# Kernel tuning notes

Measured on AMD Instinct MI355X. Metric: run time of the kernel, lower is better.

The kernel has to match this reference:

```python
import jax, jax.numpy as jnp
import numpy as np

N_NODES = 50000
N_EDGES = 600000
DIMS = [128, 128, 128]  # input_dim + hidden_dims


def setup_inputs() -> dict:
    key = jax.random.key(0)
    ks = jax.random.split(key, 8)
    node_features = jax.random.normal(ks[0], (N_NODES, DIMS[0]), dtype=jnp.float32)
    edge_index = jax.random.randint(ks[1], (2, N_EDGES), 0, N_NODES, dtype=jnp.int64)
    # GCNConv params: weight [in, out] (glorot-ish), bias [out] (zeros init in PyG; use small randn)
    W1 = jax.random.normal(ks[2], (DIMS[0], DIMS[1]), dtype=jnp.float32) / np.sqrt(DIMS[0])
    b1 = jnp.zeros((DIMS[1],), dtype=jnp.float32)
    W2 = jax.random.normal(ks[3], (DIMS[1], DIMS[2]), dtype=jnp.float32) / np.sqrt(DIMS[1])
    b2 = jnp.zeros((DIMS[2],), dtype=jnp.float32)
    return {"node_features": node_features, "edge_index": edge_index,
            "W1": W1, "b1": b1, "W2": W2, "b2": b2}


def _gcn_norm(edge_index, n_nodes):
    # Add self loops, then symmetric normalization as in PyG gcn_norm.
    loop = jnp.arange(n_nodes, dtype=edge_index.dtype)
    src = jnp.concatenate([edge_index[0], loop])  # message sources (x_j)
    dst = jnp.concatenate([edge_index[1], loop])  # aggregation targets
    deg = jax.ops.segment_sum(jnp.ones_like(dst, dtype=jnp.float32), dst,
                              num_segments=n_nodes)
    dinv = jnp.where(deg > 0, jax.lax.rsqrt(jnp.maximum(deg, 1.0)), 0.0)
    norm = dinv[src] * dinv[dst]  # [E + N]
    return src, dst, norm


def _gcn_layer(x, W, b, src, dst, norm, n_nodes):
    h = x @ W                                  # [N, out]
    msgs = h[src] * norm[:, None]              # gather + scale  [E+N, out]
    out = jax.ops.segment_sum(msgs, dst, num_segments=n_nodes)  # scatter-add
    return out + b


def reference(node_features, edge_index, W1, b1, W2, b2):
    n_nodes = node_features.shape[0]
    src, dst, norm = _gcn_norm(edge_index, n_nodes)
    x = _gcn_layer(node_features, W1, b1, src, dst, norm, n_nodes)
    x = jax.nn.relu(x)  # ReLU between layers, none after last
    x = _gcn_layer(x, W2, b2, src, dst, norm, n_nodes)
    return x
```

## Files before the change

### kernel.cpp

```cpp
#include <hip/hip_runtime.h>
#include <hip/hip_bf16.h>

typedef __bf16 bf16_t;
typedef __bf16 bf16x8 __attribute__((ext_vector_type(8)));
typedef float f32x4 __attribute__((ext_vector_type(4)));
typedef unsigned short u16;

#define DIM 128
#define CAPE 62

__global__ void k_prep(const float* __restrict__ W1, const float* __restrict__ W2,
                       bf16_t* __restrict__ TH1, bf16_t* __restrict__ TL1,
                       bf16_t* __restrict__ TH2, bf16_t* __restrict__ TL2) {
    int b = blockIdx.x;
    const float* W = (b == 0) ? W1 : W2;
    bf16_t* TH = (b == 0) ? TH1 : TH2;
    bf16_t* TL = (b == 0) ? TL1 : TL2;
    for (int idx = threadIdx.x; idx < 128 * 128; idx += 256) {
        int j    = idx & 7;
        int lane = (idx >> 3) & 63;
        int kc   = (idx >> 9) & 3;
        int nt   = idx >> 11;
        int nn = nt * 16 + (lane & 15);
        int k  = kc * 32 + (lane >> 4) * 8 + j;
        float wv = W[k * 128 + nn];
        bf16_t h = (bf16_t)wv;
        TH[idx] = h;
        TL[idx] = (bf16_t)(wv - (float)h);
    }
}

__global__ __launch_bounds__(256) void k_front(
        const bf16_t* __restrict__ TH1, const bf16_t* __restrict__ TL1,
        const float* __restrict__ A, bf16_t* __restrict__ H, int M, int SB,
        const int* __restrict__ EI, int* __restrict__ ell, int e) {
    int b = blockIdx.x;
    int tid = threadIdx.x;
    if (b < SB) {
        __shared__ int any;
        if (tid == 0) any = 0;
        __syncthreads();
        long e0 = ((long)b * 256 + tid) * 4;
        long rem = (long)e - e0;
        int ns = rem >= 4 ? 4 : (rem > 0 ? (int)rem : 0);
        int s[4] = {0, 0, 0, 0};
        int hi = 0;
        if (ns == 4) {
            int4 p0 = *(const int4*)(EI + 2 * e0);
            int4 p1 = *(const int4*)(EI + 2 * e0 + 4);
            s[0] = p0.x; s[1] = p0.z; s[2] = p1.x; s[3] = p1.z;
            hi = p0.y | p0.w | p1.y | p1.w;
        } else {
            for (int q = 0; q < ns; q++) { s[q] = EI[2 * (e0 + q)]; hi |= EI[2 * (e0 + q) + 1]; }
        }
        if (hi) atomicOr(&any, 1);
        __syncthreads();
        int d[4] = {0, 0, 0, 0};
        if (any == 0) {
            if (ns == 4) {
                int4 q0 = *(const int4*)(EI + 2 * ((long)e + e0));
                int4 q1 = *(const int4*)(EI + 2 * ((long)e + e0) + 4);
                d[0] = q0.x; d[1] = q0.z; d[2] = q1.x; d[3] = q1.z;
            } else {
                for (int q = 0; q < ns; q++) d[q] = EI[2 * ((long)e + e0 + q)];
            }
        } else {
            if (ns == 4) {
                int4 ss = *(const int4*)(EI + e0);
                s[0] = ss.x; s[1] = ss.y; s[2] = ss.z; s[3] = ss.w;
                int4 dd = *(const int4*)(EI + (long)e + e0);
                d[0] = dd.x; d[1] = dd.y; d[2] = dd.z; d[3] = dd.w;
            } else {
                for (int q = 0; q < ns; q++) { s[q] = EI[e0 + q]; d[q] = EI[(long)e + e0 + q]; }
            }
        }
        int pos[4];
#pragma unroll
        for (int q = 0; q < 4; q++)
            if (q < ns) pos[q] = atomicAdd(ell + (long)d[q] * 32 + 31, 1);
#pragma unroll
        for (int q = 0; q < 4; q++)
            if (q < ns && pos[q] < CAPE)
                ((u16*)ell)[(long)d[q] * 64 + pos[q]] = (u16)s[q];
        return;
    }
    int wave = tid >> 6, lane = tid & 63;
    long row_base = ((long)(b - SB) * 4 + wave) * 16;
    if (row_base >= M) return;
    int n16 = lane & 15, quad = lane >> 4;

    bf16x8 a_hi[4], a_lo[4];
    const float* arow = A + (row_base + n16) * DIM + quad * 8;
#pragma unroll
    for (int kc = 0; kc < 4; kc++) {
        float4 p0 = *(const float4*)(arow + kc * 32);
        float4 p1 = *(const float4*)(arow + kc * 32 + 4);
        float v[8] = {p0.x, p0.y, p0.z, p0.w, p1.x, p1.y, p1.z, p1.w};
#pragma unroll
        for (int j = 0; j < 8; j++) {
            bf16_t h = (bf16_t)v[j];
            a_hi[kc][j] = h;
            a_lo[kc][j] = (bf16_t)(v[j] - (float)h);
        }
    }
#pragma unroll
    for (int nt = 0; nt < 8; nt++) {
        f32x4 acc = {0.f, 0.f, 0.f, 0.f};
#pragma unroll
        for (int kc = 0; kc < 4; kc++) {
            long tb = ((long)(nt * 4 + kc) * 64 + lane) * 8;
            bf16x8 bh = *(const bf16x8*)(TH1 + tb);
            bf16x8 bl = *(const bf16x8*)(TL1 + tb);
            acc = __builtin_amdgcn_mfma_f32_16x16x32_bf16(a_hi[kc], bh, acc, 0, 0, 0);
            acc = __builtin_amdgcn_mfma_f32_16x16x32_bf16(a_lo[kc], bh, acc, 0, 0, 0);
            acc = __builtin_amdgcn_mfma_f32_16x16x32_bf16(a_hi[kc], bl, acc, 0, 0, 0);
        }
        bf16_t* hrow = H + (row_base + quad * 4) * DIM + nt * 16 + n16;
#pragma unroll
        for (int r = 0; r < 4; r++) hrow[(long)r * DIM] = (bf16_t)acc[r];
    }
}

__global__ void k_dinv(const int* __restrict__ ell, float* __restrict__ dinv, int n) {
    int g = blockIdx.x * 256 + threadIdx.x;
    if (g < n) dinv[g] = rsqrtf((float)(ell[(long)g * 32 + 31] + 1));
}

__global__ __launch_bounds__(256) void k_agg1(const bf16_t* __restrict__ H,
        const int* __restrict__ ell, const float* __restrict__ dinv,
        const float* __restrict__ bias, bf16_t* __restrict__ outb, int n) {
    int lane = threadIdx.x & 63;
    int wave = threadIdx.x >> 6;
    int sub = lane >> 4;
    int sl  = lane & 15;
    int i = (blockIdx.x * 4 + wave) * 4 + sub;
    bool act = (i < n);
    float acc[8] = {0.f, 0.f, 0.f, 0.f, 0.f, 0.f, 0.f, 0.f};
    float d = 0.f;
    int deg = 0;
    const u16* crow = (const u16*)ell;
    if (act) {
        d = dinv[i];
        deg = ell[(long)i * 32 + 31];
        if (deg > CAPE) deg = CAPE;
        crow = (const u16*)(ell + (long)i * 32);
        bf16x8 hs = *(const bf16x8*)(H + (long)i * DIM + sl * 8);
#pragma unroll
        for (int q = 0; q < 8; q++) acc[q] = d * (float)hs[q];
    }
    int j = 0;
    for (; j + 4 <= deg; j += 4) {
        ushort4 ss = *(const ushort4*)(crow + j);
        float w0 = dinv[ss.x], w1 = dinv[ss.y], w2 = dinv[ss.z], w3 = dinv[ss.w];
        bf16x8 h0 = *(const bf16x8*)(H + (long)ss.x * DIM + sl * 8);
        bf16x8 h1 = *(const bf16x8*)(H + (long)ss.y * DIM + sl * 8);
        bf16x8 h2 = *(const bf16x8*)(H + (long)ss.z * DIM + sl * 8);
        bf16x8 h3 = *(const bf16x8*)(H + (long)ss.w * DIM + sl * 8);
#pragma unroll
        for (int q = 0; q < 8; q++)
            acc[q] += (w0 * (float)h0[q] + w1 * (float)h1[q])
                    + (w2 * (float)h2[q] + w3 * (float)h3[q]);
    }
    for (; j < deg; j++) {
        int s0 = crow[j];
        float w0 = dinv[s0];
        bf16x8 h0 = *(const bf16x8*)(H + (long)s0 * DIM + sl * 8);
#pragma unroll
        for (int q = 0; q < 8; q++) acc[q] += w0 * (float)h0[q];
    }
    if (act) {
        float4 b0 = *(const float4*)(bias + sl * 8);
        float4 b1 = *(const float4*)(bias + sl * 8 + 4);
        float r[8];
        r[0] = d * acc[0] + b0.x; r[1] = d * acc[1] + b0.y;
        r[2] = d * acc[2] + b0.z; r[3] = d * acc[3] + b0.w;
        r[4] = d * acc[4] + b1.x; r[5] = d * acc[5] + b1.y;
        r[6] = d * acc[6] + b1.z; r[7] = d * acc[7] + b1.w;
        bf16x8 o;
#pragma unroll
        for (int q = 0; q < 8; q++) o[q] = (bf16_t)fmaxf(r[q], 0.f);
        *(bf16x8*)(outb + (long)i * DIM + sl * 8) = o;
    }
}

__global__ __launch_bounds__(256) void k_gemm_b16(const bf16_t* __restrict__ A,
        const bf16_t* __restrict__ TH, const bf16_t* __restrict__ TL,
        const float* __restrict__ dinv, bf16_t* __restrict__ H, int M) {
    int tid = threadIdx.x;
    int wave = tid >> 6, lane = tid & 63;
    long row_base = ((long)blockIdx.x * 4 + wave) * 16;
    if (row_base >= M) return;
    int n16 = lane & 15, quad = lane >> 4;

    bf16x8 a[4];
    const bf16_t* arow = A + (row_base + n16) * DIM + quad * 8;
#pragma unroll
    for (int kc = 0; kc < 4; kc++) a[kc] = *(const bf16x8*)(arow + kc * 32);

    float dr[4];
#pragma unroll
    for (int r = 0; r < 4; r++) dr[r] = dinv[row_base + quad * 4 + r];

#pragma unroll
    for (int nt = 0; nt < 8; nt++) {
        f32x4 acc = {0.f, 0.f, 0.f, 0.f};
#pragma unroll
        for (int kc = 0; kc < 4; kc++) {
            long tb = ((long)(nt * 4 + kc) * 64 + lane) * 8;
            bf16x8 bh = *(const bf16x8*)(TH + tb);
            bf16x8 bl = *(const bf16x8*)(TL + tb);
            acc = __builtin_amdgcn_mfma_f32_16x16x32_bf16(a[kc], bh, acc, 0, 0, 0);
            acc = __builtin_amdgcn_mfma_f32_16x16x32_bf16(a[kc], bl, acc, 0, 0, 0);
        }
        bf16_t* hrow = H + (row_base + quad * 4) * DIM + nt * 16 + n16;
#pragma unroll
        for (int r = 0; r < 4; r++) hrow[(long)r * DIM] = (bf16_t)(dr[r] * acc[r]);
    }
}

__global__ __launch_bounds__(256) void k_agg2(const bf16_t* __restrict__ H,
        const int* __restrict__ ell, const float* __restrict__ dinv,
        const float* __restrict__ bias, float* __restrict__ outf, int n) {
    int lane = threadIdx.x & 63;
    int wave = threadIdx.x >> 6;
    int sub = lane >> 4;
    int sl  = lane & 15;
    int i = (blockIdx.x * 4 + wave) * 4 + sub;
    bool act = (i < n);
    float acc[8] = {0.f, 0.f, 0.f, 0.f, 0.f, 0.f, 0.f, 0.f};
    float d = 0.f;
    int deg = 0;
    const u16* crow = (const u16*)ell;
    if (act) {
        d = dinv[i];
        deg = ell[(long)i * 32 + 31];
        if (deg > CAPE) deg = CAPE;
        crow = (const u16*)(ell + (long)i * 32);
        bf16x8 hs = *(const bf16x8*)(H + (long)i * DIM + sl * 8);
#pragma unroll
        for (int q = 0; q < 8; q++) acc[q] = (float)hs[q];
    }
    int j = 0;
    for (; j + 4 <= deg; j += 4) {
        ushort4 ss = *(const ushort4*)(crow + j);
        bf16x8 h0 = *(const bf16x8*)(H + (long)ss.x * DIM + sl * 8);
        bf16x8 h1 = *(const bf16x8*)(H + (long)ss.y * DIM + sl * 8);
        bf16x8 h2 = *(const bf16x8*)(H + (long)ss.z * DIM + sl * 8);
        bf16x8 h3 = *(const bf16x8*)(H + (long)ss.w * DIM + sl * 8);
#pragma unroll
        for (int q = 0; q < 8; q++)
            acc[q] += ((float)h0[q] + (float)h1[q]) + ((float)h2[q] + (float)h3[q]);
    }
    for (; j < deg; j++) {
        int s0 = crow[j];
        bf16x8 h0 = *(const bf16x8*)(H + (long)s0 * DIM + sl * 8);
#pragma unroll
        for (int q = 0; q < 8; q++) acc[q] += (float)h0[q];
    }
    if (act) {
        float4 b0 = *(const float4*)(bias + sl * 8);
        float4 b1 = *(const float4*)(bias + sl * 8 + 4);
        float* op = outf + (long)i * DIM + sl * 8;
        *(float4*)op = make_float4(d * acc[0] + b0.x, d * acc[1] + b0.y,
                                   d * acc[2] + b0.z, d * acc[3] + b0.w);
        *(float4*)(op + 4) = make_float4(d * acc[4] + b1.x, d * acc[5] + b1.y,
                                         d * acc[6] + b1.z, d * acc[7] + b1.w);
    }
}

extern "C" void kernel_launch(void* const* d_in, const int* in_sizes, int n_in,
                              void* d_out, int out_size, void* d_ws, size_t ws_size,
                              hipStream_t stream) {
    const float* X  = (const float*)d_in[0];
    const int*   EI = (const int*)d_in[1];
    const float* W1 = (const float*)d_in[2];
    const float* B1 = (const float*)d_in[3];
    const float* W2 = (const float*)d_in[4];
    const float* B2 = (const float*)d_in[5];
    float* OUT = (float*)d_out;

    const int N = in_sizes[0] / DIM;
    const int E = in_sizes[1] / 2;
    (void)n_in; (void)out_size; (void)ws_size;

    char* w = (char*)d_ws;
    auto alloc = [&](size_t bytes) -> char* {
        char* p = w;
        w += (bytes + 255) & ~(size_t)255;
        return p;
    };
    int*    ell  = (int*)alloc((size_t)N * 128);
    float*  dinv = (float*)alloc((size_t)N * 4);
    bf16_t* TH1  = (bf16_t*)alloc(128 * 128 * 2);
    bf16_t* TL1  = (bf16_t*)alloc(128 * 128 * 2);
    bf16_t* TH2  = (bf16_t*)alloc(128 * 128 * 2);
    bf16_t* TL2  = (bf16_t*)alloc(128 * 128 * 2);
    bf16_t* H1   = (bf16_t*)alloc((size_t)N * DIM * 2);
    bf16_t* H2   = (bf16_t*)alloc((size_t)N * DIM * 2);
    bf16_t* X1b  = (bf16_t*)alloc((size_t)N * DIM * 2);

    int gN = (N + 255) / 256;
    int SB = (E + 1023) / 1024;
    int GB = (N + 63) / 64;
    int gA = (N + 15) / 16;

    hipMemsetAsync(ell, 0, (size_t)N * 128, stream);
    k_prep<<<2, 256, 0, stream>>>(W1, W2, TH1, TL1, TH2, TL2);
    k_front<<<SB + GB, 256, 0, stream>>>(TH1, TL1, X, H1, N, SB, EI, ell, E);
    k_dinv<<<gN, 256, 0, stream>>>(ell, dinv, N);
    k_agg1<<<gA, 256, 0, stream>>>(H1, ell, dinv, B1, X1b, N);
    k_gemm_b16<<<GB, 256, 0, stream>>>(X1b, TH2, TL2, dinv, H2, N);
    k_agg2<<<gA, 256, 0, stream>>>(H2, ell, dinv, B2, OUT, N);
}
```

Baseline: 202.5 us.

## Fuse layer-1 aggregation with layer-2 GEMM via LDS tile, batch neighbor gathers

Merges the first aggregation kernel and the second bf16 GEMM into one kernel. Each 16-row block aggregates into a swizzled shared-memory tile and runs MFMA on it directly, so the intermediate X1b never goes to global memory and one launch is removed. Both aggregation kernels now issue up to 16 neighbor row loads at once before accumulating, to expose more memory-level parallelism. The edge-scatter front end handles 8 edges per thread instead of 4. The fused kernel drops the row bounds check, which assumes N is a multiple of 16. It also spends more registers on the batched gathers, which may lower occupancy.

```diff
diff --git a/kernel.cpp b/kernel.cpp
--- a/kernel.cpp
+++ b/kernel.cpp
@@ -40,46 +40,57 @@
         __shared__ int any;
         if (tid == 0) any = 0;
         __syncthreads();
-        long e0 = ((long)b * 256 + tid) * 4;
+        long e0 = ((long)b * 256 + tid) * 8;
         long rem = (long)e - e0;
-        int ns = rem >= 4 ? 4 : (rem > 0 ? (int)rem : 0);
-        int s[4] = {0, 0, 0, 0};
+        int ns = rem >= 8 ? 8 : (rem > 0 ? (int)rem : 0);
+        int s[8], d[8];
         int hi = 0;
-        if (ns == 4) {
+        if (ns == 8) {
             int4 p0 = *(const int4*)(EI + 2 * e0);
             int4 p1 = *(const int4*)(EI + 2 * e0 + 4);
+            int4 p2 = *(const int4*)(EI + 2 * e0 + 8);
+            int4 p3 = *(const int4*)(EI + 2 * e0 + 12);
             s[0] = p0.x; s[1] = p0.z; s[2] = p1.x; s[3] = p1.z;
-            hi = p0.y | p0.w | p1.y | p1.w;
+            s[4] = p2.x; s[5] = p2.z; s[6] = p3.x; s[7] = p3.z;
+            hi = (p0.y | p0.w) | (p1.y | p1.w) | (p2.y | p2.w) | (p3.y | p3.w);
         } else {
+            for (int q = 0; q < 8; q++) s[q] = 0;
             for (int q = 0; q < ns; q++) { s[q] = EI[2 * (e0 + q)]; hi |= EI[2 * (e0 + q) + 1]; }
         }
         if (hi) atomicOr(&any, 1);
         __syncthreads();
-        int d[4] = {0, 0, 0, 0};
+        for (int q = 0; q < 8; q++) d[q] = 0;
         if (any == 0) {
-            if (ns == 4) {
+            if (ns == 8) {
                 int4 q0 = *(const int4*)(EI + 2 * ((long)e + e0));
                 int4 q1 = *(const int4*)(EI + 2 * ((long)e + e0) + 4);
+                int4 q2 = *(const int4*)(EI + 2 * ((long)e + e0) + 8);
+                int4 q3 = *(const int4*)(EI + 2 * ((long)e + e0) + 12);
                 d[0] = q0.x; d[1] = q0.z; d[2] = q1.x; d[3] = q1.z;
+                d[4] = q2.x; d[5] = q2.z; d[6] = q3.x; d[7] = q3.z;
             } else {
                 for (int q = 0; q < ns; q++) d[q] = EI[2 * ((long)e + e0 + q)];
             }
         } else {
-            if (ns == 4) {
-                int4 ss = *(const int4*)(EI + e0);
-                s[0] = ss.x; s[1] = ss.y; s[2] = ss.z; s[3] = ss.w;
-                int4 dd = *(const int4*)(EI + (long)e + e0);
-                d[0] = dd.x; d[1] = dd.y; d[2] = dd.z; d[3] = dd.w;
+            if (ns == 8) {
+                int4 s0 = *(const int4*)(EI + e0);
+                int4 s1 = *(const int4*)(EI + e0 + 4);
+                s[0] = s0.x; s[1] = s0.y; s[2] = s0.z; s[3] = s0.w;
+                s[4] = s1.x; s[5] = s1.y; s[6] = s1.z; s[7] = s1.w;
+                int4 d0 = *(const int4*)(EI + (long)e + e0);
+                int4 d1 = *(const int4*)(EI + (long)e + e0 + 4);
+                d[0] = d0.x; d[1] = d0.y; d[2] = d0.z; d[3] = d0.w;
+                d[4] = d1.x; d[5] = d1.y; d[6] = d1.z; d[7] = d1.w;
             } else {
                 for (int q = 0; q < ns; q++) { s[q] = EI[e0 + q]; d[q] = EI[(long)e + e0 + q]; }
             }
         }
-        int pos[4];
-#pragma unroll
-        for (int q = 0; q < 4; q++)
+        int pos[8];
+#pragma unroll
+        for (int q = 0; q < 8; q++)
             if (q < ns) pos[q] = atomicAdd(ell + (long)d[q] * 32 + 31, 1);
 #pragma unroll
-        for (int q = 0; q < 4; q++)
+        for (int q = 0; q < 8; q++)
             if (q < ns && pos[q] < CAPE)
                 ((u16*)ell)[(long)d[q] * 64 + pos[q]] = (u16)s[q];
         return;
@@ -126,49 +137,59 @@
     if (g < n) dinv[g] = rsqrtf((float)(ell[(long)g * 32 + 31] + 1));
 }
 
-__global__ __launch_bounds__(256) void k_agg1(const bf16_t* __restrict__ H,
+__global__ __launch_bounds__(256) void k_aggemm(const bf16_t* __restrict__ H,
         const int* __restrict__ ell, const float* __restrict__ dinv,
-        const float* __restrict__ bias, bf16_t* __restrict__ outb, int n) {
+        const float* __restrict__ bias,
+        const bf16_t* __restrict__ TH, const bf16_t* __restrict__ TL,
+        bf16_t* __restrict__ H2, int n) {
+    __shared__ bf16_t tile[16 * 128];
+    __shared__ float sdinv[16];
     int lane = threadIdx.x & 63;
     int wave = threadIdx.x >> 6;
     int sub = lane >> 4;
     int sl  = lane & 15;
-    int i = (blockIdx.x * 4 + wave) * 4 + sub;
-    bool act = (i < n);
-    float acc[8] = {0.f, 0.f, 0.f, 0.f, 0.f, 0.f, 0.f, 0.f};
-    float d = 0.f;
-    int deg = 0;
-    const u16* crow = (const u16*)ell;
-    if (act) {
-        d = dinv[i];
-        deg = ell[(long)i * 32 + 31];
-        if (deg > CAPE) deg = CAPE;
-        crow = (const u16*)(ell + (long)i * 32);
-        bf16x8 hs = *(const bf16x8*)(H + (long)i * DIM + sl * 8);
+    int lr  = wave * 4 + sub;
+    long i  = (long)blockIdx.x * 16 + lr;
+
+    float d = dinv[i];
+    int deg = ell[i * 32 + 31];
+    if (deg > CAPE) deg = CAPE;
+    const u16* crow = (const u16*)(ell + i * 32);
+    float acc[8];
+    {
+        bf16x8 hs = *(const bf16x8*)(H + i * DIM + sl * 8);
 #pragma unroll
         for (int q = 0; q < 8; q++) acc[q] = d * (float)hs[q];
     }
-    int j = 0;
-    for (; j + 4 <= deg; j += 4) {
-        ushort4 ss = *(const ushort4*)(crow + j);
-        float w0 = dinv[ss.x], w1 = dinv[ss.y], w2 = dinv[ss.z], w3 = dinv[ss.w];
-        bf16x8 h0 = *(const bf16x8*)(H + (long)ss.x * DIM + sl * 8);
-        bf16x8 h1 = *(const bf16x8*)(H + (long)ss.y * DIM + sl * 8);
-        bf16x8 h2 = *(const bf16x8*)(H + (long)ss.z * DIM + sl * 8);
-        bf16x8 h3 = *(const bf16x8*)(H + (long)ss.w * DIM + sl * 8);
-#pragma unroll
-        for (int q = 0; q < 8; q++)
-            acc[q] += (w0 * (float)h0[q] + w1 * (float)h1[q])
-                    + (w2 * (float)h2[q] + w3 * (float)h3[q]);
-    }
-    for (; j < deg; j++) {
+    ushort4 c0 = ((const ushort4*)crow)[0];
+    ushort4 c1 = ((const ushort4*)crow)[1];
+    ushort4 c2 = ((const ushort4*)crow)[2];
+    ushort4 c3 = ((const ushort4*)crow)[3];
+    u16 cols[16] = {c0.x, c0.y, c0.z, c0.w, c1.x, c1.y, c1.z, c1.w,
+                    c2.x, c2.y, c2.z, c2.w, c3.x, c3.y, c3.z, c3.w};
+    bf16x8 hv[16];
+    float wv[16];
+#pragma unroll
+    for (int j = 0; j < 16; j++)
+        if (j < deg) {
+            int s0 = cols[j];
+            wv[j] = dinv[s0];
+            hv[j] = *(const bf16x8*)(H + (long)s0 * DIM + sl * 8);
+        }
+#pragma unroll
+    for (int j = 0; j < 16; j++)
+        if (j < deg) {
+#pragma unroll
+            for (int q = 0; q < 8; q++) acc[q] += wv[j] * (float)hv[j][q];
+        }
+    for (int j = 16; j < deg; j++) {
         int s0 = crow[j];
         float w0 = dinv[s0];
         bf16x8 h0 = *(const bf16x8*)(H + (long)s0 * DIM + sl * 8);
 #pragma unroll
         for (int q = 0; q < 8; q++) acc[q] += w0 * (float)h0[q];
     }
-    if (act) {
+    {
         float4 b0 = *(const float4*)(bias + sl * 8);
         float4 b1 = *(const float4*)(bias + sl * 8 + 4);
         float r[8];
@@ -179,42 +200,38 @@
         bf16x8 o;
 #pragma unroll
         for (int q = 0; q < 8; q++) o[q] = (bf16_t)fmaxf(r[q], 0.f);
-        *(bf16x8*)(outb + (long)i * DIM + sl * 8) = o;
-    }
-}
-
-__global__ __launch_bounds__(256) void k_gemm_b16(const bf16_t* __restrict__ A,
-        const bf16_t* __restrict__ TH, const bf16_t* __restrict__ TL,
-        const float* __restrict__ dinv, bf16_t* __restrict__ H, int M) {
-    int tid = threadIdx.x;
-    int wave = tid >> 6, lane = tid & 63;
-    long row_base = ((long)blockIdx.x * 4 + wave) * 16;
-    if (row_base >= M) return;
-    int n16 = lane & 15, quad = lane >> 4;
-
+        int off = lr * 256 + ((sl * 16) ^ ((lr & 7) << 4));
+        *(bf16x8*)((char*)tile + off) = o;
+        if (sl == 0) sdinv[lr] = d;
+    }
+    __syncthreads();
+
+    int n16 = sl, quad = sub;
     bf16x8 a[4];
-    const bf16_t* arow = A + (row_base + n16) * DIM + quad * 8;
-#pragma unroll
-    for (int kc = 0; kc < 4; kc++) a[kc] = *(const bf16x8*)(arow + kc * 32);
-
+#pragma unroll
+    for (int kc = 0; kc < 4; kc++) {
+        int off = n16 * 256 + (((kc * 64 + quad * 16)) ^ ((n16 & 7) << 4));
+        a[kc] = *(const bf16x8*)((char*)tile + off);
+    }
     float dr[4];
 #pragma unroll
-    for (int r = 0; r < 4; r++) dr[r] = dinv[row_base + quad * 4 + r];
-
-#pragma unroll
-    for (int nt = 0; nt < 8; nt++) {
-        f32x4 acc = {0.f, 0.f, 0.f, 0.f};
+    for (int r = 0; r < 4; r++) dr[r] = sdinv[quad * 4 + r];
+    long row_base = (long)blockIdx.x * 16;
+#pragma unroll
+    for (int t = 0; t < 2; t++) {
+        int nt = wave * 2 + t;
+        f32x4 acc2 = {0.f, 0.f, 0.f, 0.f};
 #pragma unroll
         for (int kc = 0; kc < 4; kc++) {
             long tb = ((long)(nt * 4 + kc) * 64 + lane) * 8;
             bf16x8 bh = *(const bf16x8*)(TH + tb);
             bf16x8 bl = *(const bf16x8*)(TL + tb);
-            acc = __builtin_amdgcn_mfma_f32_16x16x32_bf16(a[kc], bh, acc, 0, 0, 0);
-            acc = __builtin_amdgcn_mfma_f32_16x16x32_bf16(a[kc], bl, acc, 0, 0, 0);
-        }
-        bf16_t* hrow = H + (row_base + quad * 4) * DIM + nt * 16 + n16;
-#pragma unroll
-        for (int r = 0; r < 4; r++) hrow[(long)r * DIM] = (bf16_t)(dr[r] * acc[r]);
+            acc2 = __builtin_amdgcn_mfma_f32_16x16x32_bf16(a[kc], bh, acc2, 0, 0, 0);
+            acc2 = __builtin_amdgcn_mfma_f32_16x16x32_bf16(a[kc], bl, acc2, 0, 0, 0);
+        }
+        bf16_t* hrow = H2 + (row_base + quad * 4) * DIM + nt * 16 + n16;
+#pragma unroll
+        for (int r = 0; r < 4; r++) hrow[(long)r * DIM] = (bf16_t)(dr[r] * acc2[r]);
     }
 }
 
@@ -225,42 +242,44 @@
     int wave = threadIdx.x >> 6;
     int sub = lane >> 4;
     int sl  = lane & 15;
-    int i = (blockIdx.x * 4 + wave) * 4 + sub;
-    bool act = (i < n);
-    float acc[8] = {0.f, 0.f, 0.f, 0.f, 0.f, 0.f, 0.f, 0.f};
-    float d = 0.f;
-    int deg = 0;
-    const u16* crow = (const u16*)ell;
-    if (act) {
-        d = dinv[i];
-        deg = ell[(long)i * 32 + 31];
-        if (deg > CAPE) deg = CAPE;
-        crow = (const u16*)(ell + (long)i * 32);
-        bf16x8 hs = *(const bf16x8*)(H + (long)i * DIM + sl * 8);
+    long i = (long)(blockIdx.x * 4 + wave) * 4 + sub;
+    if (i >= n) return;
+    float d = dinv[i];
+    int deg = ell[i * 32 + 31];
+    if (deg > CAPE) deg = CAPE;
+    const u16* crow = (const u16*)(ell + i * 32);
+    float acc[8];
+    {
+        bf16x8 hs = *(const bf16x8*)(H + i * DIM + sl * 8);
 #pragma unroll
         for (int q = 0; q < 8; q++) acc[q] = (float)hs[q];
     }
-    int j = 0;
-    for (; j + 4 <= deg; j += 4) {
-        ushort4 ss = *(const ushort4*)(crow + j);
-        bf16x8 h0 = *(const bf16x8*)(H + (long)ss.x * DIM + sl * 8);
-        bf16x8 h1 = *(const bf16x8*)(H + (long)ss.y * DIM + sl * 8);
-        bf16x8 h2 = *(const bf16x8*)(H + (long)ss.z * DIM + sl * 8);
-        bf16x8 h3 = *(const bf16x8*)(H + (long)ss.w * DIM + sl * 8);
-#pragma unroll
-        for (int q = 0; q < 8; q++)
-            acc[q] += ((float)h0[q] + (float)h1[q]) + ((float)h2[q] + (float)h3[q]);
-    }
-    for (; j < deg; j++) {
+    ushort4 c0 = ((const ushort4*)crow)[0];
+    ushort4 c1 = ((const ushort4*)crow)[1];
+    ushort4 c2 = ((const ushort4*)crow)[2];
+    ushort4 c3 = ((const ushort4*)crow)[3];
+    u16 cols[16] = {c0.x, c0.y, c0.z, c0.w, c1.x, c1.y, c1.z, c1.w,
+                    c2.x, c2.y, c2.z, c2.w, c3.x, c3.y, c3.z, c3.w};
+    bf16x8 hv[16];
+#pragma unroll
+    for (int j = 0; j < 16; j++)
+        if (j < deg) hv[j] = *(const bf16x8*)(H + (long)cols[j] * DIM + sl * 8);
+#pragma unroll
+    for (int j = 0; j < 16; j++)
+        if (j < deg) {
+#pragma unroll
+            for (int q = 0; q < 8; q++) acc[q] += (float)hv[j][q];
+        }
+    for (int j = 16; j < deg; j++) {
         int s0 = crow[j];
         bf16x8 h0 = *(const bf16x8*)(H + (long)s0 * DIM + sl * 8);
 #pragma unroll
         for (int q = 0; q < 8; q++) acc[q] += (float)h0[q];
     }
-    if (act) {
+    {
         float4 b0 = *(const float4*)(bias + sl * 8);
         float4 b1 = *(const float4*)(bias + sl * 8 + 4);
-        float* op = outf + (long)i * DIM + sl * 8;
+        float* op = outf + i * DIM + sl * 8;
         *(float4*)op = make_float4(d * acc[0] + b0.x, d * acc[1] + b0.y,
                                    d * acc[2] + b0.z, d * acc[3] + b0.w);
         *(float4*)(op + 4) = make_float4(d * acc[4] + b1.x, d * acc[5] + b1.y,
@@ -297,18 +316,16 @@
     bf16_t* TL2  = (bf16_t*)alloc(128 * 128 * 2);
     bf16_t* H1   = (bf16_t*)alloc((size_t)N * DIM * 2);
     bf16_t* H2   = (bf16_t*)alloc((size_t)N * DIM * 2);
-    bf16_t* X1b  = (bf16_t*)alloc((size_t)N * DIM * 2);
 
     int gN = (N + 255) / 256;
-    int SB = (E + 1023) / 1024;
+    int SB = (E + 2047) / 2048;
     int GB = (N + 63) / 64;
-    int gA = (N + 15) / 16;
+    int gT = (N + 15) / 16;
 
     hipMemsetAsync(ell, 0, (size_t)N * 128, stream);
     k_prep<<<2, 256, 0, stream>>>(W1, W2, TH1, TL1, TH2, TL2);
     k_front<<<SB + GB, 256, 0, stream>>>(TH1, TL1, X, H1, N, SB, EI, ell, E);
     k_dinv<<<gN, 256, 0, stream>>>(ell, dinv, N);
-    k_agg1<<<gA, 256, 0, stream>>>(H1, ell, dinv, B1, X1b, N);
-    k_gemm_b16<<<GB, 256, 0, stream>>>(X1b, TH2, TL2, dinv, H2, N);
-    k_agg2<<<gA, 256, 0, stream>>>(H2, ell, dinv, B2, OUT, N);
-}
+    k_aggemm<<<gT, 256, 0, stream>>>(H1, ell, dinv, B1, TH2, TL2, H2, N);
+    k_agg2<<<gT, 256, 0, stream>>>(H2, ell, dinv, B2, OUT, N);
+}
```

Measured after the change: 195.4 us. 3.5% less time.
